# Optimization experiments

Hardware: AMD Instinct MI355X
Metric: run time of the kernel (lower is better)

## Reference

```python
import jax, jax.numpy as jnp
import numpy as np

N_HEADS = 4
N_HIDDEN = 64  # out_features (concat=False)
MASK_FILL = -9e15
ADJ_THRESH = 0.05


def setup_inputs() -> dict:
    key = jax.random.key(0)
    k1, k2, k3, k4 = jax.random.split(key, 4)
    B, S, N, F = 32, 20, 128, 64
    h = jax.random.normal(k1, (B, S, N, F), dtype=jnp.float32)
    adj_mat = jax.random.uniform(k2, (B, S, N, N), dtype=jnp.float32)
    W = jax.random.normal(k3, (F, N_HEADS * N_HIDDEN), dtype=jnp.float32) * (1.0 / np.sqrt(F))
    a = jax.random.normal(k4, (N_HEADS, 2 * N_HIDDEN, 1), dtype=jnp.float32) * 0.1
    return {"h": h, "adj_mat": adj_mat, "W": W, "a": a}


def reference(h, adj_mat, W, a):
    B, S, N, _ = h.shape
    # Linear projection (no bias); dropout is a no-op (training=False)
    ht = jnp.einsum('bsnf,fo->bsno', h, W)
    # (B, S, H, N, D)
    ht = ht.reshape(B, S, N, N_HEADS, N_HIDDEN).transpose(0, 1, 3, 2, 4)
    a_src = a[:, :N_HIDDEN, 0]   # (H, D)
    a_tgt = a[:, N_HIDDEN:, 0]   # (H, D)
    src = jnp.einsum('bshnd,hd->bshn', ht, a_src)  # (B,S,H,N)
    tgt = jnp.einsum('bshnd,hd->bshn', ht, a_tgt)
    # additive sigmoid score: e_ij = sigmoid(src_i + tgt_j)
    e = jax.nn.sigmoid(src[..., :, None] + tgt[..., None, :])  # (B,S,H,N,N)
    mask = (adj_mat < ADJ_THRESH)[:, :, None, :, :]  # broadcast over heads
    e = jnp.where(mask, MASK_FILL, e)
    attn = jax.nn.softmax(e, axis=-1)
    h_prime = jnp.einsum('bshij,bshjd->bshid', attn, ht)
    # concat=False -> mean over heads
    return h_prime.mean(axis=2)  # (B,S,N,D)
```

## Files before the change

kernel.cpp:

```cpp
#include <hip/hip_runtime.h>
#include <hip/hip_bf16.h>

#define ADJ_TH 0.05f

typedef __bf16 bf16x8 __attribute__((ext_vector_type(8)));
typedef __bf16 bf16x4 __attribute__((ext_vector_type(4)));
typedef float  f32x4  __attribute__((ext_vector_type(4)));

__global__ void wt_convert_kernel(const float* __restrict__ W, __bf16* __restrict__ Wt) {
    int id = blockIdx.x * 256 + threadIdx.x;
    int o = id >> 6, k = id & 63;
    Wt[o * 64 + k] = (__bf16)W[k * 256 + o];
}

__global__ __launch_bounds__(256)
void mask_build_kernel(const float* __restrict__ adj, unsigned* __restrict__ mws) {
    int bs = blockIdx.x, tid = threadIdx.x;
    const float* ab = adj + (size_t)bs * 128 * 128;
    #pragma unroll
    for (int rp = 0; rp < 2; ++rp) {
        int widx = tid + rp * 256;
        int i = widx >> 2, wq = widx & 3;
        const float4* ap = reinterpret_cast<const float4*>(ab + i * 128 + wq * 32);
        unsigned bits = 0u;
        #pragma unroll
        for (int v = 0; v < 8; ++v) {
            float4 f = ap[v];
            bits |= (f.x < ADJ_TH ? 1u : 0u) << (4 * v + 0);
            bits |= (f.y < ADJ_TH ? 1u : 0u) << (4 * v + 1);
            bits |= (f.z < ADJ_TH ? 1u : 0u) << (4 * v + 2);
            bits |= (f.w < ADJ_TH ? 1u : 0u) << (4 * v + 3);
        }
        mws[(bs * 128 + i) * 4 + wq] = bits;
    }
}

__device__ __forceinline__ int sw_idx(int o, int i) {
    return o * 128 + ((((i >> 3) ^ o) & 15) << 3) + (i & 7);
}

template<bool WSMASK>
__global__ __launch_bounds__(256, 3)
void gat_main_kernel(const float* __restrict__ hg, const float* __restrict__ adj,
                     const float* __restrict__ ag, const __bf16* __restrict__ Wt,
                     const unsigned* __restrict__ mws, float* __restrict__ out)
{
    const int bs  = blockIdx.x;
    const int tid = threadIdx.x;
    const int w   = tid >> 6;
    const int l   = tid & 63;
    const int l15 = l & 15;
    const int l4  = l >> 4;

    __shared__ __bf16   ht_t[128 * 128];
    __shared__ float    src_sh[2][128], tgt_sh[2][128];
    __shared__ unsigned mask_sh[WSMASK ? 4 : 512];

    const float* hb = hg + (size_t)bs * 128 * 64;

    uint4 mq[2];
    if constexpr (WSMASK) {
        #pragma unroll
        for (int m2 = 0; m2 < 2; ++m2) {
            int irow = 16 * (2 * w + m2) + l15;
            mq[m2] = *reinterpret_cast<const uint4*>(mws + ((size_t)bs * 128 + irow) * 4);
        }
    } else {
        const float* ab = adj + (size_t)bs * 128 * 128;
        #pragma unroll
        for (int rp = 0; rp < 2; ++rp) {
            int widx = tid + rp * 256;
            int i = widx >> 2, wq = widx & 3;
            const float4* ap = reinterpret_cast<const float4*>(ab + i * 128 + wq * 32);
            unsigned bits = 0u;
            #pragma unroll
            for (int v = 0; v < 8; ++v) {
                float4 f = ap[v];
                bits |= (f.x < ADJ_TH ? 1u : 0u) << (4 * v + 0);
                bits |= (f.y < ADJ_TH ? 1u : 0u) << (4 * v + 1);
                bits |= (f.z < ADJ_TH ? 1u : 0u) << (4 * v + 2);
                bits |= (f.w < ADJ_TH ? 1u : 0u) << (4 * v + 3);
            }
            mask_sh[i * 4 + wq] = bits;
        }
    }

    bf16x8 af[2][2];
    #pragma unroll
    for (int m2 = 0; m2 < 2; ++m2) {
        int row = 16 * (2 * w + m2) + l15;
        #pragma unroll
        for (int ks = 0; ks < 2; ++ks) {
            const float4* p4 = reinterpret_cast<const float4*>(hb + row * 64 + 8 * l4 + 32 * ks);
            float4 lo = p4[0], hi = p4[1];
            bf16x8 v;
            v[0]=(__bf16)lo.x; v[1]=(__bf16)lo.y; v[2]=(__bf16)lo.z; v[3]=(__bf16)lo.w;
            v[4]=(__bf16)hi.x; v[5]=(__bf16)hi.y; v[6]=(__bf16)hi.z; v[7]=(__bf16)hi.w;
            af[m2][ks] = v;
        }
    }

    f32x4 acc2[2][4];
    #pragma unroll
    for (int m2 = 0; m2 < 2; ++m2)
        #pragma unroll
        for (int nt = 0; nt < 4; ++nt) { f32x4 z = {0.f,0.f,0.f,0.f}; acc2[m2][nt] = z; }

    #pragma unroll 1
    for (int p = 0; p < 2; ++p) {
        #pragma unroll 1
        for (int hg2 = 0; hg2 < 2; ++hg2) {
            int h = 2 * p + hg2;
            float ps[2][4], pt[2][4];
            #pragma unroll
            for (int m2 = 0; m2 < 2; ++m2)
                #pragma unroll
                for (int r = 0; r < 4; ++r) { ps[m2][r] = 0.f; pt[m2][r] = 0.f; }

            #pragma unroll
            for (int nq = 0; nq < 4; ++nq) {
                int nt   = 4 * hg2 + nq;
                int oloc = 16 * nt + l15;
                int og   = 128 * p + oloc;
                int d    = 16 * nq + l15;
                float a_s = ag[h * 128 + d];
                float a_t = ag[h * 128 + 64 + d];
                bf16x8 b0 = *reinterpret_cast<const bf16x8*>(Wt + og * 64 + 8 * l4);
                bf16x8 b1 = *reinterpret_cast<const bf16x8*>(Wt + og * 64 + 8 * l4 + 32);
                #pragma unroll
                for (int m2 = 0; m2 < 2; ++m2) {
                    f32x4 acc = {0.f,0.f,0.f,0.f};
                    acc = __builtin_amdgcn_mfma_f32_16x16x32_bf16(af[m2][0], b0, acc, 0,0,0);
                    acc = __builtin_amdgcn_mfma_f32_16x16x32_bf16(af[m2][1], b1, acc, 0,0,0);
                    int i0 = 16 * (2 * w + m2) + 4 * l4;
                    bf16x4 st;
                    st[0]=(__bf16)acc[0]; st[1]=(__bf16)acc[1];
                    st[2]=(__bf16)acc[2]; st[3]=(__bf16)acc[3];
                    *reinterpret_cast<bf16x4*>(&ht_t[sw_idx(oloc, i0)]) = st;
                    #pragma unroll
                    for (int r = 0; r < 4; ++r) {
                        ps[m2][r] += acc[r] * a_s;
                        pt[m2][r] += acc[r] * a_t;
                    }
                }
            }
            #pragma unroll
            for (int s = 1; s < 16; s <<= 1)
                #pragma unroll
                for (int m2 = 0; m2 < 2; ++m2)
                    #pragma unroll
                    for (int r = 0; r < 4; ++r) {
                        ps[m2][r] += __shfl_xor(ps[m2][r], s);
                        pt[m2][r] += __shfl_xor(pt[m2][r], s);
                    }
            if (l15 == 0) {
                #pragma unroll
                for (int m2 = 0; m2 < 2; ++m2)
                    #pragma unroll
                    for (int r = 0; r < 4; ++r) {
                        int i = 16 * (2 * w + m2) + 4 * l4 + r;
                        src_sh[hg2][i] = ps[m2][r];
                        tgt_sh[hg2][i] = pt[m2][r];
                    }
            }
        }
        __syncthreads();

        #pragma unroll 1
        for (int hp = 0; hp < 2; ++hp) {
            bf16x8 pa[2][4];
            #pragma unroll
            for (int m2 = 0; m2 < 2; ++m2) {
                int irow = 16 * (2 * w + m2) + l15;
                float si = src_sh[hp][irow];
                unsigned mw[4];
                if constexpr (WSMASK) {
                    mw[0]=mq[m2].x; mw[1]=mq[m2].y; mw[2]=mq[m2].z; mw[3]=mq[m2].w;
                } else {
                    uint4 t = *reinterpret_cast<const uint4*>(&mask_sh[irow * 4]);
                    mw[0]=t.x; mw[1]=t.y; mw[2]=t.z; mw[3]=t.w;
                }

                float pf[4][8];
                float dloc = 0.f;
                #pragma unroll
                for (int ks = 0; ks < 4; ++ks) {
                    const float4* tp = reinterpret_cast<const float4*>(&tgt_sh[hp][8 * l4 + 32 * ks]);
                    float4 t0 = tp[0], t1 = tp[1];
                    float tg[8] = {t0.x,t0.y,t0.z,t0.w,t1.x,t1.y,t1.z,t1.w};
                    #pragma unroll
                    for (int e = 0; e < 8; ++e) {
                        float x  = si + tg[e];
                        float sg = __builtin_amdgcn_rcpf(1.0f + __expf(-x));
                        float pe = __expf(sg);
                        float pv = ((mw[ks] >> (8 * l4 + e)) & 1u) ? 0.f : pe;
                        pf[ks][e] = pv;
                        dloc += pv;
                    }
                }
                dloc += __shfl_xor(dloc, 16);
                dloc += __shfl_xor(dloc, 32);
                float scale = 0.25f * __builtin_amdgcn_rcpf(fmaxf(dloc, 1e-20f));

                #pragma unroll
                for (int ks = 0; ks < 4; ++ks) {
                    bf16x8 v;
                    #pragma unroll
                    for (int e = 0; e < 8; ++e) v[e] = (__bf16)(pf[ks][e] * scale);
                    pa[m2][ks] = v;
                }
            }

            #pragma unroll
            for (int nt = 0; nt < 4; ++nt) {
                #pragma unroll
                for (int ks = 0; ks < 4; ++ks) {
                    bf16x8 b = *reinterpret_cast<const bf16x8*>(
                        &ht_t[sw_idx(64 * hp + 16 * nt + l15, 8 * l4 + 32 * ks)]);
                    acc2[0][nt] = __builtin_amdgcn_mfma_f32_16x16x32_bf16(pa[0][ks], b, acc2[0][nt], 0,0,0);
                    acc2[1][nt] = __builtin_amdgcn_mfma_f32_16x16x32_bf16(pa[1][ks], b, acc2[1][nt], 0,0,0);
                }
            }
        }
        __syncthreads();
    }

    float* ob = out + (size_t)bs * 128 * 64;
    #pragma unroll
    for (int m2 = 0; m2 < 2; ++m2)
        #pragma unroll
        for (int nt = 0; nt < 4; ++nt)
            #pragma unroll
            for (int r = 0; r < 4; ++r)
                ob[(32 * w + 16 * m2 + 4 * l4 + r) * 64 + 16 * nt + l15] = acc2[m2][nt][r];
}

extern "C" void kernel_launch(void* const* d_in, const int* in_sizes, int n_in,
                              void* d_out, int out_size, void* d_ws, size_t ws_size,
                              hipStream_t stream) {
    const float* h   = (const float*)d_in[0];
    const float* adj = (const float*)d_in[1];
    const float* W   = (const float*)d_in[2];
    const float* a   = (const float*)d_in[3];
    float* out = (float*)d_out;

    __bf16*   Wt  = (__bf16*)d_ws;
    unsigned* mws = (unsigned*)((char*)d_ws + 65536);
    const size_t need = 65536 + (size_t)640 * 128 * 4 * sizeof(unsigned);

    wt_convert_kernel<<<64, 256, 0, stream>>>(W, Wt);
    if (ws_size >= need) {
        mask_build_kernel<<<640, 256, 0, stream>>>(adj, mws);
        gat_main_kernel<true><<<640, 256, 0, stream>>>(h, adj, a, Wt, mws, out);
    } else {
        gat_main_kernel<false><<<640, 256, 0, stream>>>(h, adj, a, Wt, mws, out);
    }
}
```

Before: 140.8 us.

## Precompute W·a projections, fuse mask build via ballot, and reorder head pipeline

Folds the attention vectors into the weights (W·a_src, W·a_tgt) in a small prep kernel, so each block gets the src/tgt scores for all four heads from one pair of MFMAs instead of per-head shuffle reductions. The separate mask-build kernel and its workspace round trip are replaced by an in-kernel ballot over adj rows written to shared memory. The head loop is restructured so the softmax for one head is computed before the projection GEMM writes ht, and the second head's softmax comes before both aggregation GEMMs, which may overlap VALU and MFMA work. The folded scores are formed from bf16 WA and bf16 h, which changes rounding compared with the previous path.

```diff
diff --git a/kernel.cpp b/kernel.cpp
--- a/kernel.cpp
+++ b/kernel.cpp
@@ -7,31 +7,28 @@
 typedef __bf16 bf16x4 __attribute__((ext_vector_type(4)));
 typedef float  f32x4  __attribute__((ext_vector_type(4)));
 
-__global__ void wt_convert_kernel(const float* __restrict__ W, __bf16* __restrict__ Wt) {
-    int id = blockIdx.x * 256 + threadIdx.x;
-    int o = id >> 6, k = id & 63;
-    Wt[o * 64 + k] = (__bf16)W[k * 256 + o];
-}
-
 __global__ __launch_bounds__(256)
-void mask_build_kernel(const float* __restrict__ adj, unsigned* __restrict__ mws) {
-    int bs = blockIdx.x, tid = threadIdx.x;
-    const float* ab = adj + (size_t)bs * 128 * 128;
-    #pragma unroll
-    for (int rp = 0; rp < 2; ++rp) {
-        int widx = tid + rp * 256;
-        int i = widx >> 2, wq = widx & 3;
-        const float4* ap = reinterpret_cast<const float4*>(ab + i * 128 + wq * 32);
-        unsigned bits = 0u;
-        #pragma unroll
-        for (int v = 0; v < 8; ++v) {
-            float4 f = ap[v];
-            bits |= (f.x < ADJ_TH ? 1u : 0u) << (4 * v + 0);
-            bits |= (f.y < ADJ_TH ? 1u : 0u) << (4 * v + 1);
-            bits |= (f.z < ADJ_TH ? 1u : 0u) << (4 * v + 2);
-            bits |= (f.w < ADJ_TH ? 1u : 0u) << (4 * v + 3);
-        }
-        mws[(bs * 128 + i) * 4 + wq] = bits;
+void prep_kernel(const float* __restrict__ W, const float* __restrict__ a,
+                 __bf16* __restrict__ Wt, __bf16* __restrict__ WAt) {
+    const int t = threadIdx.x;
+    if (blockIdx.x == 0) {
+        #pragma unroll 4
+        for (int r = 0; r < 64; ++r) {
+            int id = r * 256 + t;
+            Wt[(id & 255) * 64 + (id >> 8)] = (__bf16)W[id];
+        }
+    } else {
+        for (int id = t; id < 1024; id += 256) {
+            int n = id >> 6, f = id & 63;
+            float s = 0.f;
+            if (n < 8) {
+                int hh = n >> 1, st = n & 1;
+                #pragma unroll 8
+                for (int d = 0; d < 64; ++d)
+                    s += W[f * 256 + hh * 64 + d] * a[hh * 128 + st * 64 + d];
+            }
+            WAt[n * 64 + f] = (__bf16)s;
+        }
     }
 }
 
@@ -39,11 +36,10 @@
     return o * 128 + ((((i >> 3) ^ o) & 15) << 3) + (i & 7);
 }
 
-template<bool WSMASK>
 __global__ __launch_bounds__(256, 3)
 void gat_main_kernel(const float* __restrict__ hg, const float* __restrict__ adj,
-                     const float* __restrict__ ag, const __bf16* __restrict__ Wt,
-                     const unsigned* __restrict__ mws, float* __restrict__ out)
+                     const __bf16* __restrict__ Wt, const __bf16* __restrict__ WAt,
+                     float* __restrict__ out)
 {
     const int bs  = blockIdx.x;
     const int tid = threadIdx.x;
@@ -53,36 +49,19 @@
     const int l4  = l >> 4;
 
     __shared__ __bf16   ht_t[128 * 128];
-    __shared__ float    src_sh[2][128], tgt_sh[2][128];
-    __shared__ unsigned mask_sh[WSMASK ? 4 : 512];
-
-    const float* hb = hg + (size_t)bs * 128 * 64;
-
-    uint4 mq[2];
-    if constexpr (WSMASK) {
-        #pragma unroll
-        for (int m2 = 0; m2 < 2; ++m2) {
-            int irow = 16 * (2 * w + m2) + l15;
-            mq[m2] = *reinterpret_cast<const uint4*>(mws + ((size_t)bs * 128 + irow) * 4);
-        }
-    } else {
-        const float* ab = adj + (size_t)bs * 128 * 128;
-        #pragma unroll
-        for (int rp = 0; rp < 2; ++rp) {
-            int widx = tid + rp * 256;
-            int i = widx >> 2, wq = widx & 3;
-            const float4* ap = reinterpret_cast<const float4*>(ab + i * 128 + wq * 32);
-            unsigned bits = 0u;
-            #pragma unroll
-            for (int v = 0; v < 8; ++v) {
-                float4 f = ap[v];
-                bits |= (f.x < ADJ_TH ? 1u : 0u) << (4 * v + 0);
-                bits |= (f.y < ADJ_TH ? 1u : 0u) << (4 * v + 1);
-                bits |= (f.z < ADJ_TH ? 1u : 0u) << (4 * v + 2);
-                bits |= (f.w < ADJ_TH ? 1u : 0u) << (4 * v + 3);
-            }
-            mask_sh[i * 4 + wq] = bits;
-        }
+    __shared__ float    src_sh[4][128];
+    __shared__ float    tgt_sh[4][128];
+    __shared__ unsigned mask_sh[512];
+
+    const float* hb = hg  + (size_t)bs * 8192;
+    const float* ab = adj + (size_t)bs * 16384;
+
+    #pragma unroll 8
+    for (int it = 0; it < 64; ++it) {
+        int row = 32 * w + (it >> 1);
+        int col = ((it & 1) << 6) + l;
+        unsigned long long bal = __ballot(ab[row * 128 + col] < ADJ_TH);
+        if (l < 2) mask_sh[row * 4 + ((it & 1) << 1) + l] = (unsigned)(bal >> (32 * l));
     }
 
     bf16x8 af[2][2];
@@ -100,132 +79,115 @@
         }
     }
 
+    {
+        bf16x8 wa0 = *reinterpret_cast<const bf16x8*>(WAt + l15 * 64 + 8 * l4);
+        bf16x8 wa1 = *reinterpret_cast<const bf16x8*>(WAt + l15 * 64 + 8 * l4 + 32);
+        #pragma unroll
+        for (int m2 = 0; m2 < 2; ++m2) {
+            f32x4 acc = {0.f,0.f,0.f,0.f};
+            acc = __builtin_amdgcn_mfma_f32_16x16x32_bf16(af[m2][0], wa0, acc, 0,0,0);
+            acc = __builtin_amdgcn_mfma_f32_16x16x32_bf16(af[m2][1], wa1, acc, 0,0,0);
+            if (l15 < 8) {
+                int hh = l15 >> 1;
+                float* dst = (l15 & 1) ? tgt_sh[hh] : src_sh[hh];
+                int i0 = 16 * (2 * w + m2) + 4 * l4;
+                #pragma unroll
+                for (int r = 0; r < 4; ++r) dst[i0 + r] = acc[r];
+            }
+        }
+    }
+    __syncthreads();
+
     f32x4 acc2[2][4];
     #pragma unroll
     for (int m2 = 0; m2 < 2; ++m2)
         #pragma unroll
         for (int nt = 0; nt < 4; ++nt) { f32x4 z = {0.f,0.f,0.f,0.f}; acc2[m2][nt] = z; }
 
+    auto compute_pa = [&](int hh, bf16x8 (&pa)[2][4]) {
+        #pragma unroll
+        for (int m2 = 0; m2 < 2; ++m2) {
+            int irow = 16 * (2 * w + m2) + l15;
+            float si = src_sh[hh][irow];
+            uint4 mm = *reinterpret_cast<const uint4*>(&mask_sh[irow * 4]);
+            unsigned mw[4] = {mm.x, mm.y, mm.z, mm.w};
+            float pf[4][8];
+            float dloc = 0.f;
+            #pragma unroll
+            for (int ks = 0; ks < 4; ++ks) {
+                const float4* tp = reinterpret_cast<const float4*>(&tgt_sh[hh][8 * l4 + 32 * ks]);
+                float4 t0 = tp[0], t1 = tp[1];
+                float tg[8] = {t0.x,t0.y,t0.z,t0.w,t1.x,t1.y,t1.z,t1.w};
+                #pragma unroll
+                for (int e = 0; e < 8; ++e) {
+                    float x  = si + tg[e];
+                    float sg = __builtin_amdgcn_rcpf(1.0f + __expf(-x));
+                    float pe = __expf(sg);
+                    float pv = ((mw[ks] >> (8 * l4 + e)) & 1u) ? 0.f : pe;
+                    pf[ks][e] = pv;
+                    dloc += pv;
+                }
+            }
+            dloc += __shfl_xor(dloc, 16);
+            dloc += __shfl_xor(dloc, 32);
+            float scale = 0.25f * __builtin_amdgcn_rcpf(fmaxf(dloc, 1e-20f));
+            #pragma unroll
+            for (int ks = 0; ks < 4; ++ks) {
+                bf16x8 v;
+                #pragma unroll
+                for (int e = 0; e < 8; ++e) v[e] = (__bf16)(pf[ks][e] * scale);
+                pa[m2][ks] = v;
+            }
+        }
+    };
+
+    auto gemm2 = [&](int hp, bf16x8 (&pa)[2][4]) {
+        #pragma unroll
+        for (int nt = 0; nt < 4; ++nt)
+            #pragma unroll
+            for (int ks = 0; ks < 4; ++ks) {
+                bf16x8 b = *reinterpret_cast<const bf16x8*>(
+                    &ht_t[sw_idx(64 * hp + 16 * nt + l15, 8 * l4 + 32 * ks)]);
+                acc2[0][nt] = __builtin_amdgcn_mfma_f32_16x16x32_bf16(pa[0][ks], b, acc2[0][nt], 0,0,0);
+                acc2[1][nt] = __builtin_amdgcn_mfma_f32_16x16x32_bf16(pa[1][ks], b, acc2[1][nt], 0,0,0);
+            }
+    };
+
     #pragma unroll 1
     for (int p = 0; p < 2; ++p) {
-        #pragma unroll 1
-        for (int hg2 = 0; hg2 < 2; ++hg2) {
-            int h = 2 * p + hg2;
-            float ps[2][4], pt[2][4];
-            #pragma unroll
-            for (int m2 = 0; m2 < 2; ++m2)
-                #pragma unroll
-                for (int r = 0; r < 4; ++r) { ps[m2][r] = 0.f; pt[m2][r] = 0.f; }
-
-            #pragma unroll
-            for (int nq = 0; nq < 4; ++nq) {
-                int nt   = 4 * hg2 + nq;
-                int oloc = 16 * nt + l15;
-                int og   = 128 * p + oloc;
-                int d    = 16 * nq + l15;
-                float a_s = ag[h * 128 + d];
-                float a_t = ag[h * 128 + 64 + d];
-                bf16x8 b0 = *reinterpret_cast<const bf16x8*>(Wt + og * 64 + 8 * l4);
-                bf16x8 b1 = *reinterpret_cast<const bf16x8*>(Wt + og * 64 + 8 * l4 + 32);
-                #pragma unroll
-                for (int m2 = 0; m2 < 2; ++m2) {
-                    f32x4 acc = {0.f,0.f,0.f,0.f};
-                    acc = __builtin_amdgcn_mfma_f32_16x16x32_bf16(af[m2][0], b0, acc, 0,0,0);
-                    acc = __builtin_amdgcn_mfma_f32_16x16x32_bf16(af[m2][1], b1, acc, 0,0,0);
-                    int i0 = 16 * (2 * w + m2) + 4 * l4;
-                    bf16x4 st;
-                    st[0]=(__bf16)acc[0]; st[1]=(__bf16)acc[1];
-                    st[2]=(__bf16)acc[2]; st[3]=(__bf16)acc[3];
-                    *reinterpret_cast<bf16x4*>(&ht_t[sw_idx(oloc, i0)]) = st;
-                    #pragma unroll
-                    for (int r = 0; r < 4; ++r) {
-                        ps[m2][r] += acc[r] * a_s;
-                        pt[m2][r] += acc[r] * a_t;
-                    }
-                }
-            }
-            #pragma unroll
-            for (int s = 1; s < 16; s <<= 1)
-                #pragma unroll
-                for (int m2 = 0; m2 < 2; ++m2)
-                    #pragma unroll
-                    for (int r = 0; r < 4; ++r) {
-                        ps[m2][r] += __shfl_xor(ps[m2][r], s);
-                        pt[m2][r] += __shfl_xor(pt[m2][r], s);
-                    }
-            if (l15 == 0) {
-                #pragma unroll
-                for (int m2 = 0; m2 < 2; ++m2)
-                    #pragma unroll
-                    for (int r = 0; r < 4; ++r) {
-                        int i = 16 * (2 * w + m2) + 4 * l4 + r;
-                        src_sh[hg2][i] = ps[m2][r];
-                        tgt_sh[hg2][i] = pt[m2][r];
-                    }
+        bf16x8 pa0[2][4];
+        compute_pa(2 * p, pa0);
+
+        #pragma unroll
+        for (int nt = 0; nt < 8; ++nt) {
+            int oloc = 16 * nt + l15;
+            const __bf16* wp = Wt + (size_t)(128 * p + oloc) * 64 + 8 * l4;
+            bf16x8 b0 = *reinterpret_cast<const bf16x8*>(wp);
+            bf16x8 b1 = *reinterpret_cast<const bf16x8*>(wp + 32);
+            #pragma unroll
+            for (int m2 = 0; m2 < 2; ++m2) {
+                f32x4 acc = {0.f,0.f,0.f,0.f};
+                acc = __builtin_amdgcn_mfma_f32_16x16x32_bf16(af[m2][0], b0, acc, 0,0,0);
+                acc = __builtin_amdgcn_mfma_f32_16x16x32_bf16(af[m2][1], b1, acc, 0,0,0);
+                int i0 = 16 * (2 * w + m2) + 4 * l4;
+                bf16x4 st;
+                st[0]=(__bf16)acc[0]; st[1]=(__bf16)acc[1];
+                st[2]=(__bf16)acc[2]; st[3]=(__bf16)acc[3];
+                *reinterpret_cast<bf16x4*>(&ht_t[sw_idx(oloc, i0)]) = st;
             }
         }
         __syncthreads();
 
-        #pragma unroll 1
-        for (int hp = 0; hp < 2; ++hp) {
-            bf16x8 pa[2][4];
-            #pragma unroll
-            for (int m2 = 0; m2 < 2; ++m2) {
-                int irow = 16 * (2 * w + m2) + l15;
-                float si = src_sh[hp][irow];
-                unsigned mw[4];
-                if constexpr (WSMASK) {
-                    mw[0]=mq[m2].x; mw[1]=mq[m2].y; mw[2]=mq[m2].z; mw[3]=mq[m2].w;
-                } else {
-                    uint4 t = *reinterpret_cast<const uint4*>(&mask_sh[irow * 4]);
-                    mw[0]=t.x; mw[1]=t.y; mw[2]=t.z; mw[3]=t.w;
-                }
-
-                float pf[4][8];
-                float dloc = 0.f;
-                #pragma unroll
-                for (int ks = 0; ks < 4; ++ks) {
-                    const float4* tp = reinterpret_cast<const float4*>(&tgt_sh[hp][8 * l4 + 32 * ks]);
-                    float4 t0 = tp[0], t1 = tp[1];
-                    float tg[8] = {t0.x,t0.y,t0.z,t0.w,t1.x,t1.y,t1.z,t1.w};
-                    #pragma unroll
-                    for (int e = 0; e < 8; ++e) {
-                        float x  = si + tg[e];
-                        float sg = __builtin_amdgcn_rcpf(1.0f + __expf(-x));
-                        float pe = __expf(sg);
-                        float pv = ((mw[ks] >> (8 * l4 + e)) & 1u) ? 0.f : pe;
-                        pf[ks][e] = pv;
-                        dloc += pv;
-                    }
-                }
-                dloc += __shfl_xor(dloc, 16);
-                dloc += __shfl_xor(dloc, 32);
-                float scale = 0.25f * __builtin_amdgcn_rcpf(fmaxf(dloc, 1e-20f));
-
-                #pragma unroll
-                for (int ks = 0; ks < 4; ++ks) {
-                    bf16x8 v;
-                    #pragma unroll
-                    for (int e = 0; e < 8; ++e) v[e] = (__bf16)(pf[ks][e] * scale);
-                    pa[m2][ks] = v;
-                }
-            }
-
-            #pragma unroll
-            for (int nt = 0; nt < 4; ++nt) {
-                #pragma unroll
-                for (int ks = 0; ks < 4; ++ks) {
-                    bf16x8 b = *reinterpret_cast<const bf16x8*>(
-                        &ht_t[sw_idx(64 * hp + 16 * nt + l15, 8 * l4 + 32 * ks)]);
-                    acc2[0][nt] = __builtin_amdgcn_mfma_f32_16x16x32_bf16(pa[0][ks], b, acc2[0][nt], 0,0,0);
-                    acc2[1][nt] = __builtin_amdgcn_mfma_f32_16x16x32_bf16(pa[1][ks], b, acc2[1][nt], 0,0,0);
-                }
-            }
+        {
+            bf16x8 pa1[2][4];
+            compute_pa(2 * p + 1, pa1);
+            gemm2(0, pa0);
+            gemm2(1, pa1);
         }
         __syncthreads();
     }
 
-    float* ob = out + (size_t)bs * 128 * 64;
+    float* ob = out + (size_t)bs * 8192;
     #pragma unroll
     for (int m2 = 0; m2 < 2; ++m2)
         #pragma unroll
@@ -244,15 +206,9 @@
     const float* a   = (const float*)d_in[3];
     float* out = (float*)d_out;
 
-    __bf16*   Wt  = (__bf16*)d_ws;
-    unsigned* mws = (unsigned*)((char*)d_ws + 65536);
-    const size_t need = 65536 + (size_t)640 * 128 * 4 * sizeof(unsigned);
-
-    wt_convert_kernel<<<64, 256, 0, stream>>>(W, Wt);
-    if (ws_size >= need) {
-        mask_build_kernel<<<640, 256, 0, stream>>>(adj, mws);
-        gat_main_kernel<true><<<640, 256, 0, stream>>>(h, adj, a, Wt, mws, out);
-    } else {
-        gat_main_kernel<false><<<640, 256, 0, stream>>>(h, adj, a, Wt, mws, out);
-    }
-}
+    __bf16* Wt  = (__bf16*)d_ws;
+    __bf16* WAt = (__bf16*)((char*)d_ws + 32768);
+
+    prep_kernel<<<2, 256, 0, stream>>>(W, a, Wt, WAt);
+    gat_main_kernel<<<640, 256, 0, stream>>>(h, adj, Wt, WAt, out);
+}
```

Result: slower. 180.3 us (+28.0%).
